# Kernel tuning notes

Hardware: AMD Instinct MI355X
Metric: run time of the kernel (lower is better)

The kernel has to match this reference:

```python
import jax, jax.numpy as jnp
import numpy as np

NUM_FREQ = 4
MAX_FREQ_LOG2 = 10.0
# standard NeRF frequency bands: 2^linspace(0, max_freq_log2, num_freq)
FREQ_BANDS = 2.0 ** np.linspace(0.0, MAX_FREQ_LOG2, NUM_FREQ).astype(np.float32)


def positional_encoding(x):
    # x: [N, 3] -> [N, 3*(1 + 2*num_freq)] = [N, 27]
    xf = x[..., None, :] * jnp.asarray(FREQ_BANDS, dtype=x.dtype)[:, None]  # [N, F, 3]
    enc = jnp.concatenate([jnp.sin(xf), jnp.cos(xf)], axis=-1)  # [N, F, 6]
    return jnp.concatenate([x, enc.reshape(x.shape[0], -1)], axis=-1)


def setup_inputs() -> dict:
    key = jax.random.key(0)
    k1, k2, k3 = jax.random.split(key, 3)
    N = 2097152
    x = jax.random.normal(k1, (N, 3), dtype=jnp.float32)
    in_dim, hidden = 27, 32
    # torch Linear default init scale ~ 1/sqrt(fan_in)
    W1 = jax.random.normal(k2, (in_dim, hidden), dtype=jnp.float32) / np.sqrt(in_dim)
    b1 = jnp.zeros((hidden,), dtype=jnp.float32)
    W2 = jax.random.normal(k3, (hidden, 1), dtype=jnp.float32) / np.sqrt(hidden)
    b2 = jnp.zeros((1,), dtype=jnp.float32)
    return {"x": x, "W1": W1, "b1": b1, "W2": W2, "b2": b2}


def reference(x, W1, b1, W2, b2):
    t = positional_encoding(x)                    # [N, 27]
    h = jax.nn.relu(t @ W1 + b1)                  # [N, 32]
    out = jax.nn.relu(h @ W2 + b2)                # [N, 1]
    return out
```

## Files before the change

### kernel.cpp

```cpp
#include <hip/hip_runtime.h>


#define NPTS  2097152
#define BLOCK 1024
#define TILES 4
#define NBLK  (NPTS / (64 * (BLOCK / 64) * TILES))
#define TABN  1024

typedef __bf16 bf16x8 __attribute__((ext_vector_type(8)));
typedef __bf16 bf16x2 __attribute__((ext_vector_type(2)));
typedef float  f32x8  __attribute__((ext_vector_type(8)));
typedef float  f32x16 __attribute__((ext_vector_type(16)));
typedef float  f32x2  __attribute__((ext_vector_type(2)));
typedef unsigned int u32;
typedef u32 u32x4 __attribute__((ext_vector_type(4)));

__global__ __launch_bounds__(BLOCK, 2) void nerf_32x32c(
    const float* __restrict__ x,
    const float* __restrict__ W1,
    const float* __restrict__ b1,
    const float* __restrict__ W2,
    const float* __restrict__ b2,
    float* __restrict__ out)
{
    __shared__ u32 stab[TABN];
    __shared__ __align__(16) float ws[928];

    const int tid  = threadIdx.x;
    const int wave = tid >> 6;
    const int lane = tid & 63;
    const int h    = lane >> 5;
    const int col  = lane & 31;

    if (tid < 232) {
        float4 v;
        if (tid < 216)      v = ((const float4*)W1)[tid];
        else if (tid < 224) v = ((const float4*)b1)[tid - 216];
        else                v = ((const float4*)W2)[tid - 224];
        ((float4*)ws)[tid] = v;
    }
    if (tid < TABN) {
        const float a = (float)tid * (1.0f / TABN);
        f32x2 sc;
        sc[0] = __builtin_amdgcn_sinf(a);
        sc[1] = __builtin_amdgcn_cosf(a);
        stab[tid] = __builtin_bit_cast(u32, __builtin_convertvector(sc, bf16x2));
    }

    const float C4 = 0.15915494309189535f * (float)TABN * 4.0f;
    const float FgA = (h ? 10.0793684f : 1.0f)         * C4;
    const float FgB = (h ? 1024.0f     : 101.5936673f) * C4;
    const float bias2 = b2[0];
    const f32x16 Z = {};

    __syncthreads();

    bf16x8 af1, af2;
    {
        f32x8 t1, t2;
        #pragma unroll
        for (int m = 0; m < 3; ++m) {
            t1[2 * m]     = ws[(3  + 6 * h + m) * 32 + col];
            t1[2 * m + 1] = ws[(6  + 6 * h + m) * 32 + col];
            t2[2 * m]     = ws[(15 + 6 * h + m) * 32 + col];
            t2[2 * m + 1] = ws[(18 + 6 * h + m) * 32 + col];
        }
        t1[6] = h ? ws[2 * 32 + col] : ws[0 * 32 + col];
        t1[7] = h ? ws[864 + col]    : ws[1 * 32 + col];
        t2[6] = 0.0f; t2[7] = 0.0f;
        af1 = __builtin_convertvector(t1, bf16x8);
        af2 = __builtin_convertvector(t2, bf16x8);
    }
    f32x2 w2p[8];
    #pragma unroll
    for (int m = 0; m < 8; ++m) {
        const int r0 = 896 + 8 * (m >> 1) + 4 * h + 2 * (m & 1);
        w2p[m][0] = ws[r0];
        w2p[m][1] = ws[r0 + 1];
    }

    const char* stabB = (const char*)stab;
    const int tbase = blockIdx.x * ((BLOCK / 64) * TILES) + wave * TILES;
    const float* xb = x + (size_t)tbase * 192 + col * 3;
    float* ob = out + (size_t)tbase * 64 + lane;

    #pragma unroll
    for (int t = 0; t < TILES; ++t) {
        float S[2];
        #pragma unroll
        for (int gr = 0; gr < 2; ++gr) {
            const float x0 = xb[t * 192 + gr * 96 + 0];
            const float x1 = xb[t * 192 + gr * 96 + 1];
            const float x2 = xb[t * 192 + gr * 96 + 2];

            const u32 mA0 = (u32)(int)(x0 * FgA) & (4 * (TABN - 1));
            const u32 mA1 = (u32)(int)(x1 * FgA) & (4 * (TABN - 1));
            const u32 mA2 = (u32)(int)(x2 * FgA) & (4 * (TABN - 1));
            const u32 mB0 = (u32)(int)(x0 * FgB) & (4 * (TABN - 1));
            const u32 mB1 = (u32)(int)(x1 * FgB) & (4 * (TABN - 1));
            const u32 mB2 = (u32)(int)(x2 * FgB) & (4 * (TABN - 1));

            u32x4 u1, u2;
            u1[0] = *(const u32*)(stabB + mA0);
            u1[1] = *(const u32*)(stabB + mA1);
            u1[2] = *(const u32*)(stabB + mA2);
            f32x2 ex;
            ex[0] = h ? x2 : x0;
            ex[1] = h ? 1.0f : x1;
            u1[3] = __builtin_bit_cast(u32, __builtin_convertvector(ex, bf16x2));
            u2[0] = *(const u32*)(stabB + mB0);
            u2[1] = *(const u32*)(stabB + mB1);
            u2[2] = *(const u32*)(stabB + mB2);
            u2[3] = 0u;
            const bf16x8 B1 = __builtin_bit_cast(bf16x8, u1);
            const bf16x8 B2 = __builtin_bit_cast(bf16x8, u2);

            f32x16 acc = __builtin_amdgcn_mfma_f32_32x32x16_bf16(af1, B1, Z, 0, 0, 0);
            acc = __builtin_amdgcn_mfma_f32_32x32x16_bf16(af2, B2, acc, 0, 0, 0);

            f32x2 ps = {0.0f, 0.0f};
            #pragma unroll
            for (int m = 0; m < 8; ++m) {
                f32x2 v = {acc[2 * m], acc[2 * m + 1]};
                f32x2 zz = {0.f, 0.f};
                v = __builtin_elementwise_max(v, zz);
                ps = ps + v * w2p[m];
            }
            float s = ps[0] + ps[1];
            s += __shfl_xor(s, 32, 64);
            S[gr] = s;
        }
        const float v = h ? S[1] : S[0];
        ob[t * 64] = fmaxf(v + bias2, 0.0f);
    }
}

extern "C" void kernel_launch(void* const* d_in, const int* in_sizes, int n_in,
                              void* d_out, int out_size, void* d_ws, size_t ws_size,
                              hipStream_t stream) {
    const float* x  = (const float*)d_in[0];
    const float* W1 = (const float*)d_in[1];
    const float* b1 = (const float*)d_in[2];
    const float* W2 = (const float*)d_in[3];
    const float* b2 = (const float*)d_in[4];
    float* out = (float*)d_out;

    nerf_32x32c<<<NBLK, BLOCK, 0, stream>>>(x, W1, b1, W2, b2, out);
}
```

Baseline: 18.02 us.

## Replace LDS sin/cos lookup table with direct hardware sin/cos evaluation

Removes the per-block shared-memory sin/cos table and the weight staging in LDS. Each sample now computes sin and cos directly with hardware transcendental instructions on the fractional angle, and weights are read straight from global memory. This drops the __syncthreads barrier and table setup, and block size is halved with higher occupancy bounds. The cost is 12 extra transcendental ops per point-pair in place of LDS gathers, though accuracy may improve because the table quantisation is gone.

```diff
diff --git a/kernel.cpp b/kernel.cpp
--- a/kernel.cpp
+++ b/kernel.cpp
@@ -2,10 +2,9 @@
 
 
 #define NPTS  2097152
-#define BLOCK 1024
+#define BLOCK 512
 #define TILES 4
 #define NBLK  (NPTS / (64 * (BLOCK / 64) * TILES))
-#define TABN  1024
 
 typedef __bf16 bf16x8 __attribute__((ext_vector_type(8)));
 typedef __bf16 bf16x2 __attribute__((ext_vector_type(2)));
@@ -15,7 +14,15 @@
 typedef unsigned int u32;
 typedef u32 u32x4 __attribute__((ext_vector_type(4)));
 
-__global__ __launch_bounds__(BLOCK, 2) void nerf_32x32c(
+__device__ __forceinline__ u32 pk_sc(float ang ) {
+    const float a = __builtin_amdgcn_fractf(ang);
+    f32x2 sc;
+    sc[0] = __builtin_amdgcn_sinf(a);
+    sc[1] = __builtin_amdgcn_cosf(a);
+    return __builtin_bit_cast(u32, __builtin_convertvector(sc, bf16x2));
+}
+
+__global__ __launch_bounds__(BLOCK, 4) void nerf_nolds(
     const float* __restrict__ x,
     const float* __restrict__ W1,
     const float* __restrict__ b1,
@@ -23,50 +30,30 @@
     const float* __restrict__ b2,
     float* __restrict__ out)
 {
-    __shared__ u32 stab[TABN];
-    __shared__ __align__(16) float ws[928];
-
     const int tid  = threadIdx.x;
     const int wave = tid >> 6;
     const int lane = tid & 63;
     const int h    = lane >> 5;
     const int col  = lane & 31;
 
-    if (tid < 232) {
-        float4 v;
-        if (tid < 216)      v = ((const float4*)W1)[tid];
-        else if (tid < 224) v = ((const float4*)b1)[tid - 216];
-        else                v = ((const float4*)W2)[tid - 224];
-        ((float4*)ws)[tid] = v;
-    }
-    if (tid < TABN) {
-        const float a = (float)tid * (1.0f / TABN);
-        f32x2 sc;
-        sc[0] = __builtin_amdgcn_sinf(a);
-        sc[1] = __builtin_amdgcn_cosf(a);
-        stab[tid] = __builtin_bit_cast(u32, __builtin_convertvector(sc, bf16x2));
-    }
-
-    const float C4 = 0.15915494309189535f * (float)TABN * 4.0f;
-    const float FgA = (h ? 10.0793684f : 1.0f)         * C4;
-    const float FgB = (h ? 1024.0f     : 101.5936673f) * C4;
+    const float INV2PI = 0.15915494309189535f;
+    const float FgA = (h ? 10.0793684f : 1.0f)         * INV2PI;
+    const float FgB = (h ? 1024.0f     : 101.5936673f) * INV2PI;
     const float bias2 = b2[0];
     const f32x16 Z = {};
-
-    __syncthreads();
 
     bf16x8 af1, af2;
     {
         f32x8 t1, t2;
         #pragma unroll
         for (int m = 0; m < 3; ++m) {
-            t1[2 * m]     = ws[(3  + 6 * h + m) * 32 + col];
-            t1[2 * m + 1] = ws[(6  + 6 * h + m) * 32 + col];
-            t2[2 * m]     = ws[(15 + 6 * h + m) * 32 + col];
-            t2[2 * m + 1] = ws[(18 + 6 * h + m) * 32 + col];
+            t1[2 * m]     = W1[(3  + 6 * h + m) * 32 + col];
+            t1[2 * m + 1] = W1[(6  + 6 * h + m) * 32 + col];
+            t2[2 * m]     = W1[(15 + 6 * h + m) * 32 + col];
+            t2[2 * m + 1] = W1[(18 + 6 * h + m) * 32 + col];
         }
-        t1[6] = h ? ws[2 * 32 + col] : ws[0 * 32 + col];
-        t1[7] = h ? ws[864 + col]    : ws[1 * 32 + col];
+        t1[6] = h ? W1[2 * 32 + col] : W1[0 * 32 + col];
+        t1[7] = h ? b1[col]          : W1[1 * 32 + col];
         t2[6] = 0.0f; t2[7] = 0.0f;
         af1 = __builtin_convertvector(t1, bf16x8);
         af2 = __builtin_convertvector(t2, bf16x8);
@@ -74,12 +61,11 @@
     f32x2 w2p[8];
     #pragma unroll
     for (int m = 0; m < 8; ++m) {
-        const int r0 = 896 + 8 * (m >> 1) + 4 * h + 2 * (m & 1);
-        w2p[m][0] = ws[r0];
-        w2p[m][1] = ws[r0 + 1];
+        const int r0 = 8 * (m >> 1) + 4 * h + 2 * (m & 1);
+        w2p[m][0] = W2[r0];
+        w2p[m][1] = W2[r0 + 1];
     }
 
-    const char* stabB = (const char*)stab;
     const int tbase = blockIdx.x * ((BLOCK / 64) * TILES) + wave * TILES;
     const float* xb = x + (size_t)tbase * 192 + col * 3;
     float* ob = out + (size_t)tbase * 64 + lane;
@@ -93,24 +79,17 @@
             const float x1 = xb[t * 192 + gr * 96 + 1];
             const float x2 = xb[t * 192 + gr * 96 + 2];
 
-            const u32 mA0 = (u32)(int)(x0 * FgA) & (4 * (TABN - 1));
-            const u32 mA1 = (u32)(int)(x1 * FgA) & (4 * (TABN - 1));
-            const u32 mA2 = (u32)(int)(x2 * FgA) & (4 * (TABN - 1));
-            const u32 mB0 = (u32)(int)(x0 * FgB) & (4 * (TABN - 1));
-            const u32 mB1 = (u32)(int)(x1 * FgB) & (4 * (TABN - 1));
-            const u32 mB2 = (u32)(int)(x2 * FgB) & (4 * (TABN - 1));
-
             u32x4 u1, u2;
-            u1[0] = *(const u32*)(stabB + mA0);
-            u1[1] = *(const u32*)(stabB + mA1);
-            u1[2] = *(const u32*)(stabB + mA2);
+            u1[0] = pk_sc(x0 * FgA);
+            u1[1] = pk_sc(x1 * FgA);
+            u1[2] = pk_sc(x2 * FgA);
             f32x2 ex;
             ex[0] = h ? x2 : x0;
             ex[1] = h ? 1.0f : x1;
             u1[3] = __builtin_bit_cast(u32, __builtin_convertvector(ex, bf16x2));
-            u2[0] = *(const u32*)(stabB + mB0);
-            u2[1] = *(const u32*)(stabB + mB1);
-            u2[2] = *(const u32*)(stabB + mB2);
+            u2[0] = pk_sc(x0 * FgB);
+            u2[1] = pk_sc(x1 * FgB);
+            u2[2] = pk_sc(x2 * FgB);
             u2[3] = 0u;
             const bf16x8 B1 = __builtin_bit_cast(bf16x8, u1);
             const bf16x8 B2 = __builtin_bit_cast(bf16x8, u2);
@@ -145,5 +124,5 @@
     const float* b2 = (const float*)d_in[4];
     float* out = (float*)d_out;
 
-    nerf_32x32c<<<NBLK, BLOCK, 0, stream>>>(x, W1, b1, W2, b2, out);
+    nerf_nolds<<<NBLK, BLOCK, 0, stream>>>(x, W1, b1, W2, b2, out);
 }
```

Result: no change. 17.86 us, median of 2 (-0.9%).
